# Kernel optimization log

Hardware: AMD Instinct MI355X
Metric: run time of the kernel (lower is better)

## Reference

```python
import jax, jax.numpy as jnp
import numpy as np

N = 100000      # nodes
E = 1600000     # edges
G = 1000        # graphs in the batch
D_IN, D_H, D_OUT = 128, 128, 64


def setup_inputs() -> dict:
    key = jax.random.key(0)
    ks = jax.random.split(key, 8)
    x = jax.random.normal(ks[0], (N, D_IN), jnp.float32)
    edge_index = jax.random.randint(ks[1], (2, E), 0, N, dtype=jnp.int32)
    batch = jnp.sort(jax.random.randint(ks[2], (N,), 0, G, dtype=jnp.int32))
    s_in = 1.0 / np.sqrt(D_IN)
    s_h = 1.0 / np.sqrt(D_H)
    return {
        "x": x,
        "edge_index": edge_index,
        "batch": batch,
        "W_emb": jax.random.normal(ks[3], (D_IN, D_H), jnp.float32) * s_in,
        "b_emb": jnp.zeros((D_H,), jnp.float32),
        "W1": jax.random.normal(ks[4], (D_H, D_H), jnp.float32) * s_h,
        "b1": jnp.zeros((D_H,), jnp.float32),
        "W2": jax.random.normal(ks[5], (D_H, D_H), jnp.float32) * s_h,
        "b2": jnp.zeros((D_H,), jnp.float32),
        "W3": jax.random.normal(ks[6], (D_H, D_OUT), jnp.float32) * s_h,
        "b3": jnp.zeros((D_OUT,), jnp.float32),
    }


def reference(x, edge_index, batch, W_emb, b_emb, W1, b1, W2, b2, W3, b3):
    # Eval mode: dropout is identity.
    n = x.shape[0]
    src, dst = edge_index[0], edge_index[1]
    # GCN symmetric normalization with self-loops (Kipf & Welling).
    deg = jax.ops.segment_sum(jnp.ones(src.shape[0], x.dtype), dst, num_segments=n) + 1.0
    dis = jax.lax.rsqrt(deg)                 # deg^{-1/2}, [N]
    edge_norm = dis[src] * dis[dst]          # [E]
    self_norm = dis * dis                    # self-loop weight = 1/deg, [N]

    def gcn_conv(h, W, b):
        h = h @ W                                         # [N, d_out]
        agg = jax.ops.segment_sum(h[src] * edge_norm[:, None], dst, num_segments=n)
        return agg + h * self_norm[:, None] + b

    h = x @ W_emb + b_emb
    h = jax.nn.relu(gcn_conv(h, W1, b1))
    h = jax.nn.relu(gcn_conv(h, W2, b2))
    h = gcn_conv(h, W3, b3)
    # global_add_pool over graph ids
    return jax.ops.segment_sum(h, batch, num_segments=G)
```

## Files before the change

### kernel.cpp

```cpp
#include <hip/hip_runtime.h>
#include <hip/hip_bf16.h>

#define NN 100000
#define NE 1600000
#define NG 1000

typedef unsigned short u16;
typedef unsigned int u32;
typedef u16 u16x8 __attribute__((ext_vector_type(8)));
typedef u16 u16x4 __attribute__((ext_vector_type(4)));
typedef u32 u32x4 __attribute__((ext_vector_type(4)));
typedef float f32x4 __attribute__((ext_vector_type(4)));
typedef __attribute__((ext_vector_type(8))) short s16x8;
typedef __attribute__((ext_vector_type(4))) float facc4;

__device__ __forceinline__ float bf2f(u16 u) {
    union { u32 i; float f; } c; c.i = ((u32)u) << 16; return c.f;
}
__device__ __forceinline__ u16 f2bf(float f) {
    __hip_bfloat16 h = __float2bfloat16(f);
    union { __hip_bfloat16 h; u16 u; } c; c.h = h; return c.u;
}

__global__ __launch_bounds__(256) void detect_kernel(const u32* __restrict__ xr, int* __restrict__ flag) {
    __shared__ int cnt[256];
    int c = 0;
    for (int i = threadIdx.x; i < 4096; i += 256) {
        u32 e = (xr[i] >> 7) & 0xFFu;
        if (e >= 110u && e <= 135u) c++;
    }
    cnt[threadIdx.x] = c;
    __syncthreads();
    for (int o = 128; o > 0; o >>= 1) {
        if (threadIdx.x < o) cnt[threadIdx.x] += cnt[threadIdx.x + o];
        __syncthreads();
    }
    if (threadIdx.x == 0) flag[0] = (cnt[0] > 2048) ? 1 : 0;
}

__global__ __launch_bounds__(256) void cvt_x_kernel(const void* __restrict__ xr, u16* __restrict__ xb,
                                                    const int* __restrict__ flag) {
    int c = blockIdx.x * 256 + threadIdx.x;
    const int NC = NN * 128 / 8;
    if (c >= NC) return;
    u16x8 o;
    if (flag[0]) {
        o = reinterpret_cast<const u16x8*>(xr)[c];
    } else {
        f32x4 a = reinterpret_cast<const f32x4*>(xr)[c * 2];
        f32x4 b = reinterpret_cast<const f32x4*>(xr)[c * 2 + 1];
        #pragma unroll
        for (int j = 0; j < 4; ++j) { o[j] = f2bf(a[j]); o[4 + j] = f2bf(b[j]); }
    }
    reinterpret_cast<u16x8*>(xb)[c] = o;
}

__global__ __launch_bounds__(256) void cvt_wt_kernel(const void* __restrict__ wr, u16* __restrict__ wt,
                                                     int Mcols, const int* __restrict__ flag) {
    int o = blockIdx.x * 256 + threadIdx.x;
    if (o >= Mcols * 128) return;
    int n = o >> 7, k = o & 127;
    u16 v;
    if (flag[0]) v = reinterpret_cast<const u16*>(wr)[k * Mcols + n];
    else         v = f2bf(reinterpret_cast<const float*>(wr)[k * Mcols + n]);
    wt[o] = v;
}

__global__ __launch_bounds__(256) void cvt_b_kernel(const void* __restrict__ br, float* __restrict__ bf,
                                                    int nelem, const int* __restrict__ flag) {
    int i = threadIdx.x;
    if (i >= nelem) return;
    bf[i] = flag[0] ? bf2f(reinterpret_cast<const u16*>(br)[i])
                    : reinterpret_cast<const float*>(br)[i];
}

__global__ __launch_bounds__(256) void hist_kernel(const int* __restrict__ ei, int* __restrict__ counts) {
    int e = blockIdx.x * 256 + threadIdx.x;
    if (e < NE) atomicAdd(&counts[ei[NE + e]], 1);
}

__global__ __launch_bounds__(256) void dis_kernel(const int* __restrict__ counts, float* __restrict__ dis) {
    int n = blockIdx.x * 256 + threadIdx.x;
    if (n < NN) dis[n] = rsqrtf((float)counts[n] + 1.0f);
}

__global__ __launch_bounds__(256) void scan1_kernel(const int* __restrict__ counts, int* __restrict__ offs,
                                                    int* __restrict__ bsums) {
    __shared__ int sums[256];
    int tid = threadIdx.x;
    int base = blockIdx.x * 2048 + tid * 8;
    int local[8];
    int s = 0;
    #pragma unroll
    for (int i = 0; i < 8; ++i) {
        int v = (base + i < NN) ? counts[base + i] : 0;
        local[i] = s; s += v;
    }
    sums[tid] = s;
    __syncthreads();
    for (int o = 1; o < 256; o <<= 1) {
        int v = (tid >= o) ? sums[tid - o] : 0;
        __syncthreads();
        sums[tid] += v;
        __syncthreads();
    }
    int excl = sums[tid] - s;
    #pragma unroll
    for (int i = 0; i < 8; ++i)
        if (base + i < NN) offs[base + i] = excl + local[i];
    if (tid == 255) bsums[blockIdx.x] = sums[255];
}

__global__ void scan2_kernel(int* __restrict__ bsums, int nb) {
    if (threadIdx.x == 0 && blockIdx.x == 0) {
        int run = 0;
        for (int b = 0; b < nb; ++b) { int t = bsums[b]; bsums[b] = run; run += t; }
    }
}

__global__ __launch_bounds__(256) void scan3_kernel(int* __restrict__ offs, const int* __restrict__ bsums) {
    int i = blockIdx.x * 256 + threadIdx.x;
    if (i < NN) offs[i] += bsums[i >> 11];
}

__global__ __launch_bounds__(256) void scatter_kernel(const int* __restrict__ ei, const int* __restrict__ offs,
                                                      int* __restrict__ cursor, const float* __restrict__ dis,
                                                      int2* __restrict__ edges) {
    int e = blockIdx.x * 256 + threadIdx.x;
    if (e < NE) {
        int s = ei[e], d = ei[NE + e];
        int pos = offs[d] + atomicAdd(&cursor[d], 1);
        int2 pk;
        pk.x = s;
        pk.y = __float_as_int(dis[s] * dis[d]);
        edges[pos] = pk;
    }
}

template <int M>
__global__ __launch_bounds__(256) void gemm_mfma(const u16* __restrict__ Hin, const u16* __restrict__ Wt,
                                                 const float* __restrict__ bias, u16* __restrict__ Hout) {
    constexpr int LDW = 136;
    __shared__ u16 sW[M * LDW];
    int tid = threadIdx.x;
    for (int c = tid; c < M * 16; c += 256) {
        int n = c >> 4, kc = (c & 15) << 3;
        *reinterpret_cast<u16x8*>(sW + n * LDW + kc) = reinterpret_cast<const u16x8*>(Wt)[c];
    }
    __syncthreads();

    int wv = tid >> 6, lane = tid & 63;
    int m = lane & 15, quad = lane >> 4;
    int r0 = blockIdx.x * 64 + wv * 16;
    constexpr int NT = M / 16;
    facc4 acc[NT];
    #pragma unroll
    for (int t = 0; t < NT; ++t) acc[t] = (facc4){0.f, 0.f, 0.f, 0.f};

    const u16* arow = Hin + (size_t)(r0 + m) * 128 + quad * 8;
    #pragma unroll
    for (int k0 = 0; k0 < 128; k0 += 32) {
        s16x8 a = *reinterpret_cast<const s16x8*>(arow + k0);
        #pragma unroll
        for (int t = 0; t < NT; ++t) {
            s16x8 b = *reinterpret_cast<const s16x8*>(sW + (t * 16 + m) * LDW + k0 + quad * 8);
            acc[t] = __builtin_amdgcn_mfma_f32_16x16x32_bf16(a, b, acc[t], 0, 0, 0);
        }
    }

    #pragma unroll
    for (int t = 0; t < NT; ++t) {
        int col = t * 16 + m;
        float bv = bias ? bias[col] : 0.0f;
        #pragma unroll
        for (int r = 0; r < 4; ++r) {
            int orow = r0 + quad * 4 + r;
            if (orow < NN)
                Hout[(size_t)orow * M + col] = f2bf(acc[t][r] + bv);
        }
    }
}

template <int M, bool RELU>
__global__ __launch_bounds__(256) void agg_kernel(const u16* __restrict__ T, const int* __restrict__ offs,
                                                  const int* __restrict__ counts, const float* __restrict__ dis,
                                                  const int2* __restrict__ edges,
                                                  const float* __restrict__ bias, u16* __restrict__ Hout) {
    constexpr int TPN = M / 8;
    constexpr int NPB = 256 / TPN;
    int lane = threadIdx.x % TPN;
    int n = blockIdx.x * NPB + threadIdx.x / TPN;
    if (n >= NN) return;
    const u32x4* T4 = reinterpret_cast<const u32x4*>(T);

    float di = dis[n];
    float sn = di * di;
    u32x4 ts = T4[(size_t)n * TPN + lane];
    float acc[8];
    #pragma unroll
    for (int q = 0; q < 4; ++q) {
        acc[2 * q]     = bf2f((u16)(ts[q] & 0xffffu)) * sn + bias[lane * 8 + 2 * q];
        acc[2 * q + 1] = bf2f((u16)(ts[q] >> 16))     * sn + bias[lane * 8 + 2 * q + 1];
    }

    int st = offs[n], cnt = counts[n];
    int j = 0;
    for (; j + 4 <= cnt; j += 4) {
        int2 e0 = edges[st + j];
        int2 e1 = edges[st + j + 1];
        int2 e2 = edges[st + j + 2];
        int2 e3 = edges[st + j + 3];
        u32x4 g0 = T4[(size_t)e0.x * TPN + lane];
        u32x4 g1 = T4[(size_t)e1.x * TPN + lane];
        u32x4 g2 = T4[(size_t)e2.x * TPN + lane];
        u32x4 g3 = T4[(size_t)e3.x * TPN + lane];
        float w0 = __int_as_float(e0.y), w1 = __int_as_float(e1.y);
        float w2 = __int_as_float(e2.y), w3 = __int_as_float(e3.y);
        #pragma unroll
        for (int q = 0; q < 4; ++q) {
            acc[2 * q]     += bf2f((u16)(g0[q] & 0xffffu)) * w0;
            acc[2 * q + 1] += bf2f((u16)(g0[q] >> 16))     * w0;
            acc[2 * q]     += bf2f((u16)(g1[q] & 0xffffu)) * w1;
            acc[2 * q + 1] += bf2f((u16)(g1[q] >> 16))     * w1;
            acc[2 * q]     += bf2f((u16)(g2[q] & 0xffffu)) * w2;
            acc[2 * q + 1] += bf2f((u16)(g2[q] >> 16))     * w2;
            acc[2 * q]     += bf2f((u16)(g3[q] & 0xffffu)) * w3;
            acc[2 * q + 1] += bf2f((u16)(g3[q] >> 16))     * w3;
        }
    }
    for (; j < cnt; ++j) {
        int2 e = edges[st + j];
        u32x4 g = T4[(size_t)e.x * TPN + lane];
        float w = __int_as_float(e.y);
        #pragma unroll
        for (int q = 0; q < 4; ++q) {
            acc[2 * q]     += bf2f((u16)(g[q] & 0xffffu)) * w;
            acc[2 * q + 1] += bf2f((u16)(g[q] >> 16))     * w;
        }
    }

    u32x4 ov;
    #pragma unroll
    for (int q = 0; q < 4; ++q) {
        float a0 = acc[2 * q], a1 = acc[2 * q + 1];
        if (RELU) { a0 = fmaxf(a0, 0.0f); a1 = fmaxf(a1, 0.0f); }
        ov[q] = (u32)f2bf(a0) | ((u32)f2bf(a1) << 16);
    }
    reinterpret_cast<u32x4*>(Hout)[(size_t)n * TPN + lane] = ov;
}

__global__ __launch_bounds__(64) void pool_kernel(const u16* __restrict__ H, const int* __restrict__ batch,
                                                  void* __restrict__ out, const int* __restrict__ flag) {
    int g = blockIdx.x;
    int f = threadIdx.x;
    int lo = 0, hi = NN;
    while (lo < hi) { int mid = (lo + hi) >> 1; if (batch[mid] < g) lo = mid + 1; else hi = mid; }
    int lo2 = lo, hi2 = NN;
    while (lo2 < hi2) { int mid = (lo2 + hi2) >> 1; if (batch[mid] < g + 1) lo2 = mid + 1; else hi2 = mid; }
    float acc = 0.0f;
    for (int n = lo; n < lo2; ++n) acc += bf2f(H[(size_t)n * 64 + f]);
    if (flag[0]) reinterpret_cast<u16*>(out)[g * 64 + f] = f2bf(acc);
    else         reinterpret_cast<float*>(out)[g * 64 + f] = acc;
}

extern "C" void kernel_launch(void* const* d_in, const int* in_sizes, int n_in,
                              void* d_out, int out_size, void* d_ws, size_t ws_size,
                              hipStream_t stream) {
    const void* x     = d_in[0];
    const int* ei     = (const int*)d_in[1];
    const int* batch  = (const int*)d_in[2];
    const void* W_emb = d_in[3];
    const void* b_emb = d_in[4];
    const void* W1    = d_in[5];
    const void* b1    = d_in[6];
    const void* W2    = d_in[7];
    const void* b2    = d_in[8];
    const void* W3    = d_in[9];
    const void* b3    = d_in[10];

    char* p = (char*)d_ws;
    auto alloc = [&](size_t bytes) { void* r = p; p += (bytes + 255) & ~(size_t)255; return r; };
    int*   flag   = (int*)alloc(256);
    int*   counts = (int*)alloc(NN * 4);
    int*   cursor = (int*)alloc(NN * 4);
    int*   offs   = (int*)alloc(NN * 4);
    float* dis    = (float*)alloc(NN * 4);
    int*   bsums  = (int*)alloc(256 * 4);
    int2*  edges  = (int2*)alloc((size_t)NE * 8);
    u16*   wembT  = (u16*)alloc(128 * 128 * 2);
    u16*   w1T    = (u16*)alloc(128 * 128 * 2);
    u16*   w2T    = (u16*)alloc(128 * 128 * 2);
    u16*   w3T    = (u16*)alloc(64 * 128 * 2);
    float* bembF  = (float*)alloc(128 * 4);
    float* b1F    = (float*)alloc(128 * 4);
    float* b2F    = (float*)alloc(128 * 4);
    float* b3F    = (float*)alloc(64 * 4);
    u16*   hA     = (u16*)alloc((size_t)(NN + 64) * 128 * 2);
    u16*   hB     = (u16*)alloc((size_t)(NN + 64) * 128 * 2);

    hipMemsetAsync(counts, 0, NN * 4, stream);
    hipMemsetAsync(cursor, 0, NN * 4, stream);

    const int EB = (NE + 255) / 256;
    const int NB = (NN + 255) / 256;
    const int SB = (NN + 2047) / 2048;
    const int XC = (NN * 128 / 8 + 255) / 256;
    const int GB = (NN + 63) / 64;

    detect_kernel<<<1, 256, 0, stream>>>((const u32*)x, flag);
    cvt_x_kernel<<<XC, 256, 0, stream>>>(x, hB, flag);
    cvt_wt_kernel<<<64, 256, 0, stream>>>(W_emb, wembT, 128, flag);
    cvt_wt_kernel<<<64, 256, 0, stream>>>(W1, w1T, 128, flag);
    cvt_wt_kernel<<<64, 256, 0, stream>>>(W2, w2T, 128, flag);
    cvt_wt_kernel<<<32, 256, 0, stream>>>(W3, w3T, 64, flag);
    cvt_b_kernel<<<1, 256, 0, stream>>>(b_emb, bembF, 128, flag);
    cvt_b_kernel<<<1, 256, 0, stream>>>(b1, b1F, 128, flag);
    cvt_b_kernel<<<1, 256, 0, stream>>>(b2, b2F, 128, flag);
    cvt_b_kernel<<<1, 256, 0, stream>>>(b3, b3F, 64, flag);

    hist_kernel<<<EB, 256, 0, stream>>>(ei, counts);
    dis_kernel<<<NB, 256, 0, stream>>>(counts, dis);
    scan1_kernel<<<SB, 256, 0, stream>>>(counts, offs, bsums);
    scan2_kernel<<<1, 64, 0, stream>>>(bsums, SB);
    scan3_kernel<<<NB, 256, 0, stream>>>(offs, bsums);
    scatter_kernel<<<EB, 256, 0, stream>>>(ei, offs, cursor, dis, edges);

    gemm_mfma<128><<<GB, 256, 0, stream>>>(hB, wembT, bembF, hA);
    gemm_mfma<128><<<GB, 256, 0, stream>>>(hA, w1T, nullptr, hB);
    agg_kernel<128, true><<<(NN + 15) / 16, 256, 0, stream>>>(hB, offs, counts, dis, edges, b1F, hA);
    gemm_mfma<128><<<GB, 256, 0, stream>>>(hA, w2T, nullptr, hB);
    agg_kernel<128, true><<<(NN + 15) / 16, 256, 0, stream>>>(hB, offs, counts, dis, edges, b2F, hA);
    gemm_mfma<64><<<GB, 256, 0, stream>>>(hA, w3T, nullptr, hB);
    agg_kernel<64, false><<<(NN + 31) / 32, 256, 0, stream>>>(hB, offs, counts, dis, edges, b3F, hA);
    pool_kernel<<<NG, 64, 0, stream>>>(hA, batch, d_out, flag);
}
```

Measured before the change: 553.7 us.

## Merge prep kernels, store only edge sources, and fuse aggregation with next GEMM

```diff
diff --git a/kernel.cpp b/kernel.cpp
--- a/kernel.cpp
+++ b/kernel.cpp
@@ -8,7 +8,6 @@
 typedef unsigned short u16;
 typedef unsigned int u32;
 typedef u16 u16x8 __attribute__((ext_vector_type(8)));
-typedef u16 u16x4 __attribute__((ext_vector_type(4)));
 typedef u32 u32x4 __attribute__((ext_vector_type(4)));
 typedef float f32x4 __attribute__((ext_vector_type(4)));
 typedef __attribute__((ext_vector_type(8))) short s16x8;
@@ -38,54 +37,63 @@
     if (threadIdx.x == 0) flag[0] = (cnt[0] > 2048) ? 1 : 0;
 }
 
-__global__ __launch_bounds__(256) void cvt_x_kernel(const void* __restrict__ xr, u16* __restrict__ xb,
-                                                    const int* __restrict__ flag) {
-    int c = blockIdx.x * 256 + threadIdx.x;
-    const int NC = NN * 128 / 8;
-    if (c >= NC) return;
-    u16x8 o;
-    if (flag[0]) {
-        o = reinterpret_cast<const u16x8*>(xr)[c];
+#define MEGA_NB 8039
+__global__ __launch_bounds__(256) void mega_prep(
+    const void* __restrict__ x, const int* __restrict__ flag, u16* __restrict__ xb,
+    const void* __restrict__ Wemb, const void* __restrict__ W1, const void* __restrict__ W2,
+    const void* __restrict__ W3, u16* __restrict__ wembT, u16* __restrict__ w1T,
+    u16* __restrict__ w2T, u16* __restrict__ w3T,
+    const void* __restrict__ bemb, const void* __restrict__ b1, const void* __restrict__ b2,
+    const void* __restrict__ b3, float* __restrict__ bembF, float* __restrict__ b1F,
+    float* __restrict__ b2F, float* __restrict__ b3F,
+    const int* __restrict__ ei, int* __restrict__ counts)
+{
+    int b = blockIdx.x, tid = threadIdx.x;
+    int fl = flag[0];
+    if (b < 6250) {
+        if (fl) return;
+        int c = b * 256 + tid;
+        f32x4 a = reinterpret_cast<const f32x4*>(x)[c * 2];
+        f32x4 d = reinterpret_cast<const f32x4*>(x)[c * 2 + 1];
+        u16x8 o;
+        #pragma unroll
+        for (int j = 0; j < 4; ++j) { o[j] = f2bf(a[j]); o[4 + j] = f2bf(d[j]); }
+        reinterpret_cast<u16x8*>(xb)[c] = o;
+    } else if (b < 6474) {
+        int o = (b - 6250) * 256 + tid;
+        const void* src; u16* dst; int M; int ol;
+        if (o < 16384)      { src = Wemb; dst = wembT; M = 128; ol = o; }
+        else if (o < 32768) { src = W1;   dst = w1T;   M = 128; ol = o - 16384; }
+        else if (o < 49152) { src = W2;   dst = w2T;   M = 128; ol = o - 32768; }
+        else                { src = W3;   dst = w3T;   M = 64;  ol = o - 49152; }
+        int n = ol >> 7, k = ol & 127;
+        u16 v = fl ? reinterpret_cast<const u16*>(src)[k * M + n]
+                   : f2bf(reinterpret_cast<const float*>(src)[k * M + n]);
+        dst[ol] = v;
+    } else if (b < 6476) {
+        int i = (b - 6474) * 256 + tid;
+        if (i >= 448) return;
+        const void* src; float* dst; int il;
+        if (i < 128)      { src = bemb; dst = bembF; il = i; }
+        else if (i < 256) { src = b1;   dst = b1F;   il = i - 128; }
+        else if (i < 384) { src = b2;   dst = b2F;   il = i - 256; }
+        else              { src = b3;   dst = b3F;   il = i - 384; }
+        dst[il] = fl ? bf2f(reinterpret_cast<const u16*>(src)[il])
+                     : reinterpret_cast<const float*>(src)[il];
     } else {
-        f32x4 a = reinterpret_cast<const f32x4*>(xr)[c * 2];
-        f32x4 b = reinterpret_cast<const f32x4*>(xr)[c * 2 + 1];
-        #pragma unroll
-        for (int j = 0; j < 4; ++j) { o[j] = f2bf(a[j]); o[4 + j] = f2bf(b[j]); }
-    }
-    reinterpret_cast<u16x8*>(xb)[c] = o;
-}
-
-__global__ __launch_bounds__(256) void cvt_wt_kernel(const void* __restrict__ wr, u16* __restrict__ wt,
-                                                     int Mcols, const int* __restrict__ flag) {
-    int o = blockIdx.x * 256 + threadIdx.x;
-    if (o >= Mcols * 128) return;
-    int n = o >> 7, k = o & 127;
-    u16 v;
-    if (flag[0]) v = reinterpret_cast<const u16*>(wr)[k * Mcols + n];
-    else         v = f2bf(reinterpret_cast<const float*>(wr)[k * Mcols + n]);
-    wt[o] = v;
-}
-
-__global__ __launch_bounds__(256) void cvt_b_kernel(const void* __restrict__ br, float* __restrict__ bf,
-                                                    int nelem, const int* __restrict__ flag) {
-    int i = threadIdx.x;
-    if (i >= nelem) return;
-    bf[i] = flag[0] ? bf2f(reinterpret_cast<const u16*>(br)[i])
-                    : reinterpret_cast<const float*>(br)[i];
-}
-
-__global__ __launch_bounds__(256) void hist_kernel(const int* __restrict__ ei, int* __restrict__ counts) {
-    int e = blockIdx.x * 256 + threadIdx.x;
-    if (e < NE) atomicAdd(&counts[ei[NE + e]], 1);
-}
-
-__global__ __launch_bounds__(256) void dis_kernel(const int* __restrict__ counts, float* __restrict__ dis) {
-    int n = blockIdx.x * 256 + threadIdx.x;
-    if (n < NN) dis[n] = rsqrtf((float)counts[n] + 1.0f);
+        int e0 = (b - 6476) * 1024 + tid * 4;
+        if (e0 >= NE) return;
+        int4 d4 = *reinterpret_cast<const int4*>(ei + NE + e0);
+        atomicAdd(&counts[d4.x], 1);
+        atomicAdd(&counts[d4.y], 1);
+        atomicAdd(&counts[d4.z], 1);
+        atomicAdd(&counts[d4.w], 1);
+    }
 }
 
 __global__ __launch_bounds__(256) void scan1_kernel(const int* __restrict__ counts, int* __restrict__ offs,
-                                                    int* __restrict__ bsums) {
+                                                    int* __restrict__ bsums, float* __restrict__ dis,
+                                                    int* __restrict__ cursor) {
     __shared__ int sums[256];
     int tid = threadIdx.x;
     int base = blockIdx.x * 2048 + tid * 8;
@@ -93,7 +101,12 @@
     int s = 0;
     #pragma unroll
     for (int i = 0; i < 8; ++i) {
-        int v = (base + i < NN) ? counts[base + i] : 0;
+        int v = 0;
+        if (base + i < NN) {
+            v = counts[base + i];
+            dis[base + i] = rsqrtf((float)v + 1.0f);
+            cursor[base + i] = 0;
+        }
         local[i] = s; s += v;
     }
     sums[tid] = s;
@@ -111,38 +124,44 @@
     if (tid == 255) bsums[blockIdx.x] = sums[255];
 }
 
-__global__ void scan2_kernel(int* __restrict__ bsums, int nb) {
-    if (threadIdx.x == 0 && blockIdx.x == 0) {
-        int run = 0;
-        for (int b = 0; b < nb; ++b) { int t = bsums[b]; bsums[b] = run; run += t; }
-    }
-}
-
 __global__ __launch_bounds__(256) void scan3_kernel(int* __restrict__ offs, const int* __restrict__ bsums) {
+    __shared__ int addv;
     int i = blockIdx.x * 256 + threadIdx.x;
-    if (i < NN) offs[i] += bsums[i >> 11];
+    int bucket = blockIdx.x >> 3;
+    if (threadIdx.x == 0) {
+        int s = 0;
+        for (int k = 0; k < bucket; ++k) s += bsums[k];
+        addv = s;
+    }
+    __syncthreads();
+    if (i < NN) offs[i] += addv;
 }
 
 __global__ __launch_bounds__(256) void scatter_kernel(const int* __restrict__ ei, const int* __restrict__ offs,
-                                                      int* __restrict__ cursor, const float* __restrict__ dis,
-                                                      int2* __restrict__ edges) {
-    int e = blockIdx.x * 256 + threadIdx.x;
-    if (e < NE) {
-        int s = ei[e], d = ei[NE + e];
-        int pos = offs[d] + atomicAdd(&cursor[d], 1);
-        int2 pk;
-        pk.x = s;
-        pk.y = __float_as_int(dis[s] * dis[d]);
-        edges[pos] = pk;
-    }
+                                                      int* __restrict__ cursor, int* __restrict__ srcs) {
+    int t = blockIdx.x * 256 + threadIdx.x;
+    int e0 = t * 4;
+    if (e0 >= NE) return;
+    int4 s4 = *reinterpret_cast<const int4*>(ei + e0);
+    int4 d4 = *reinterpret_cast<const int4*>(ei + NE + e0);
+    int p0 = offs[d4.x] + atomicAdd(&cursor[d4.x], 1);
+    int p1 = offs[d4.y] + atomicAdd(&cursor[d4.y], 1);
+    int p2 = offs[d4.z] + atomicAdd(&cursor[d4.z], 1);
+    int p3 = offs[d4.w] + atomicAdd(&cursor[d4.w], 1);
+    srcs[p0] = s4.x;
+    srcs[p1] = s4.y;
+    srcs[p2] = s4.z;
+    srcs[p3] = s4.w;
 }
 
 template <int M>
-__global__ __launch_bounds__(256) void gemm_mfma(const u16* __restrict__ Hin, const u16* __restrict__ Wt,
+__global__ __launch_bounds__(256) void gemm_mfma(const u16* __restrict__ Hin, const u16* __restrict__ HinAlt,
+                                                 const int* __restrict__ flag, const u16* __restrict__ Wt,
                                                  const float* __restrict__ bias, u16* __restrict__ Hout) {
     constexpr int LDW = 136;
     __shared__ u16 sW[M * LDW];
     int tid = threadIdx.x;
+    const u16* A = (HinAlt != nullptr && flag[0]) ? HinAlt : Hin;
     for (int c = tid; c < M * 16; c += 256) {
         int n = c >> 4, kc = (c & 15) << 3;
         *reinterpret_cast<u16x8*>(sW + n * LDW + kc) = reinterpret_cast<const u16x8*>(Wt)[c];
@@ -152,19 +171,20 @@
     int wv = tid >> 6, lane = tid & 63;
     int m = lane & 15, quad = lane >> 4;
     int r0 = blockIdx.x * 64 + wv * 16;
+    int ar = r0 + m; if (ar >= NN) ar = NN - 1;
     constexpr int NT = M / 16;
     facc4 acc[NT];
     #pragma unroll
     for (int t = 0; t < NT; ++t) acc[t] = (facc4){0.f, 0.f, 0.f, 0.f};
 
-    const u16* arow = Hin + (size_t)(r0 + m) * 128 + quad * 8;
+    const u16* arow = A + (size_t)ar * 128 + quad * 8;
     #pragma unroll
     for (int k0 = 0; k0 < 128; k0 += 32) {
         s16x8 a = *reinterpret_cast<const s16x8*>(arow + k0);
         #pragma unroll
         for (int t = 0; t < NT; ++t) {
-            s16x8 b = *reinterpret_cast<const s16x8*>(sW + (t * 16 + m) * LDW + k0 + quad * 8);
-            acc[t] = __builtin_amdgcn_mfma_f32_16x16x32_bf16(a, b, acc[t], 0, 0, 0);
+            s16x8 bfr = *reinterpret_cast<const s16x8*>(sW + (t * 16 + m) * LDW + k0 + quad * 8);
+            acc[t] = __builtin_amdgcn_mfma_f32_16x16x32_bf16(a, bfr, acc[t], 0, 0, 0);
         }
     }
 
@@ -181,18 +201,116 @@
     }
 }
 
+template <int MOUT>
+__global__ __launch_bounds__(256) void fused_agg_gemm(const u16* __restrict__ T, const int* __restrict__ offs,
+                                                      const int* __restrict__ counts, const float* __restrict__ dis,
+                                                      const int* __restrict__ srcs, const float* __restrict__ aggbias,
+                                                      const u16* __restrict__ Wt, u16* __restrict__ Hout) {
+    constexpr int LDW = 136;
+    __shared__ u16 sW[MOUT * LDW];
+    __shared__ u16 sA[64 * LDW];
+    int tid = threadIdx.x;
+    for (int c = tid; c < MOUT * 16; c += 256) {
+        int n = c >> 4, kc = (c & 15) << 3;
+        *reinterpret_cast<u16x8*>(sW + n * LDW + kc) = reinterpret_cast<const u16x8*>(Wt)[c];
+    }
+
+    int lane = tid & 15, grp = tid >> 4;
+    const u32x4* T4 = reinterpret_cast<const u32x4*>(T);
+    for (int i = 0; i < 4; ++i) {
+        int nl = grp * 4 + i;
+        int n = blockIdx.x * 64 + nl;
+        bool valid = n < NN;
+        int nc = valid ? n : NN - 1;
+        float di = dis[nc];
+        float sn = di * di;
+        u32x4 ts = T4[(size_t)nc * 16 + lane];
+        float acc[8];
+        #pragma unroll
+        for (int q = 0; q < 4; ++q) {
+            acc[2 * q]     = bf2f((u16)(ts[q] & 0xffffu)) * sn + aggbias[lane * 8 + 2 * q];
+            acc[2 * q + 1] = bf2f((u16)(ts[q] >> 16))     * sn + aggbias[lane * 8 + 2 * q + 1];
+        }
+        int st = offs[nc], cnt = valid ? counts[nc] : 0;
+        int j = 0;
+        for (; j + 4 <= cnt; j += 4) {
+            int e0 = srcs[st + j], e1 = srcs[st + j + 1], e2 = srcs[st + j + 2], e3 = srcs[st + j + 3];
+            float w0 = dis[e0] * di, w1 = dis[e1] * di, w2 = dis[e2] * di, w3 = dis[e3] * di;
+            u32x4 g0 = T4[(size_t)e0 * 16 + lane];
+            u32x4 g1 = T4[(size_t)e1 * 16 + lane];
+            u32x4 g2 = T4[(size_t)e2 * 16 + lane];
+            u32x4 g3 = T4[(size_t)e3 * 16 + lane];
+            #pragma unroll
+            for (int q = 0; q < 4; ++q) {
+                acc[2 * q]     += bf2f((u16)(g0[q] & 0xffffu)) * w0;
+                acc[2 * q + 1] += bf2f((u16)(g0[q] >> 16))     * w0;
+                acc[2 * q]     += bf2f((u16)(g1[q] & 0xffffu)) * w1;
+                acc[2 * q + 1] += bf2f((u16)(g1[q] >> 16))     * w1;
+                acc[2 * q]     += bf2f((u16)(g2[q] & 0xffffu)) * w2;
+                acc[2 * q + 1] += bf2f((u16)(g2[q] >> 16))     * w2;
+                acc[2 * q]     += bf2f((u16)(g3[q] & 0xffffu)) * w3;
+                acc[2 * q + 1] += bf2f((u16)(g3[q] >> 16))     * w3;
+            }
+        }
+        for (; j < cnt; ++j) {
+            int e = srcs[st + j];
+            float w = dis[e] * di;
+            u32x4 g = T4[(size_t)e * 16 + lane];
+            #pragma unroll
+            for (int q = 0; q < 4; ++q) {
+                acc[2 * q]     += bf2f((u16)(g[q] & 0xffffu)) * w;
+                acc[2 * q + 1] += bf2f((u16)(g[q] >> 16))     * w;
+            }
+        }
+        u16x8 pk;
+        #pragma unroll
+        for (int q = 0; q < 4; ++q) {
+            pk[2 * q]     = f2bf(fmaxf(acc[2 * q], 0.0f));
+            pk[2 * q + 1] = f2bf(fmaxf(acc[2 * q + 1], 0.0f));
+        }
+        *reinterpret_cast<u16x8*>(sA + nl * LDW + lane * 8) = pk;
+    }
+    __syncthreads();
+
+    int wv = tid >> 6, l64 = tid & 63;
+    int m = l64 & 15, quad = l64 >> 4;
+    int r0 = blockIdx.x * 64 + wv * 16;
+    constexpr int NT = MOUT / 16;
+    facc4 gacc[NT];
+    #pragma unroll
+    for (int t = 0; t < NT; ++t) gacc[t] = (facc4){0.f, 0.f, 0.f, 0.f};
+    #pragma unroll
+    for (int k0 = 0; k0 < 128; k0 += 32) {
+        s16x8 a = *reinterpret_cast<const s16x8*>(sA + (wv * 16 + m) * LDW + k0 + quad * 8);
+        #pragma unroll
+        for (int t = 0; t < NT; ++t) {
+            s16x8 bfr = *reinterpret_cast<const s16x8*>(sW + (t * 16 + m) * LDW + k0 + quad * 8);
+            gacc[t] = __builtin_amdgcn_mfma_f32_16x16x32_bf16(a, bfr, gacc[t], 0, 0, 0);
+        }
+    }
+    #pragma unroll
+    for (int t = 0; t < NT; ++t) {
+        int col = t * 16 + m;
+        #pragma unroll
+        for (int r = 0; r < 4; ++r) {
+            int orow = r0 + quad * 4 + r;
+            if (orow < NN)
+                Hout[(size_t)orow * MOUT + col] = f2bf(gacc[t][r]);
+        }
+    }
+}
+
 template <int M, bool RELU>
 __global__ __launch_bounds__(256) void agg_kernel(const u16* __restrict__ T, const int* __restrict__ offs,
                                                   const int* __restrict__ counts, const float* __restrict__ dis,
-                                                  const int2* __restrict__ edges,
-                                                  const float* __restrict__ bias, u16* __restrict__ Hout) {
+                                                  const int* __restrict__ srcs, const float* __restrict__ bias,
+                                                  u16* __restrict__ Hout) {
     constexpr int TPN = M / 8;
     constexpr int NPB = 256 / TPN;
     int lane = threadIdx.x % TPN;
     int n = blockIdx.x * NPB + threadIdx.x / TPN;
     if (n >= NN) return;
     const u32x4* T4 = reinterpret_cast<const u32x4*>(T);
-
     float di = dis[n];
     float sn = di * di;
     u32x4 ts = T4[(size_t)n * TPN + lane];
@@ -202,20 +320,15 @@
         acc[2 * q]     = bf2f((u16)(ts[q] & 0xffffu)) * sn + bias[lane * 8 + 2 * q];
         acc[2 * q + 1] = bf2f((u16)(ts[q] >> 16))     * sn + bias[lane * 8 + 2 * q + 1];
     }
-
     int st = offs[n], cnt = counts[n];
     int j = 0;
     for (; j + 4 <= cnt; j += 4) {
-        int2 e0 = edges[st + j];
-        int2 e1 = edges[st + j + 1];
-        int2 e2 = edges[st + j + 2];
-        int2 e3 = edges[st + j + 3];
-        u32x4 g0 = T4[(size_t)e0.x * TPN + lane];
-        u32x4 g1 = T4[(size_t)e1.x * TPN + lane];
-        u32x4 g2 = T4[(size_t)e2.x * TPN + lane];
-        u32x4 g3 = T4[(size_t)e3.x * TPN + lane];
-        float w0 = __int_as_float(e0.y), w1 = __int_as_float(e1.y);
-        float w2 = __int_as_float(e2.y), w3 = __int_as_float(e3.y);
+        int e0 = srcs[st + j], e1 = srcs[st + j + 1], e2 = srcs[st + j + 2], e3 = srcs[st + j + 3];
+        float w0 = dis[e0] * di, w1 = dis[e1] * di, w2 = dis[e2] * di, w3 = dis[e3] * di;
+        u32x4 g0 = T4[(size_t)e0 * TPN + lane];
+        u32x4 g1 = T4[(size_t)e1 * TPN + lane];
+        u32x4 g2 = T4[(size_t)e2 * TPN + lane];
+        u32x4 g3 = T4[(size_t)e3 * TPN + lane];
         #pragma unroll
         for (int q = 0; q < 4; ++q) {
             acc[2 * q]     += bf2f((u16)(g0[q] & 0xffffu)) * w0;
@@ -229,16 +342,15 @@
         }
     }
     for (; j < cnt; ++j) {
-        int2 e = edges[st + j];
-        u32x4 g = T4[(size_t)e.x * TPN + lane];
-        float w = __int_as_float(e.y);
+        int e = srcs[st + j];
+        float w = dis[e] * di;
+        u32x4 g = T4[(size_t)e * TPN + lane];
         #pragma unroll
         for (int q = 0; q < 4; ++q) {
             acc[2 * q]     += bf2f((u16)(g[q] & 0xffffu)) * w;
             acc[2 * q + 1] += bf2f((u16)(g[q] >> 16))     * w;
         }
     }
-
     u32x4 ov;
     #pragma unroll
     for (int q = 0; q < 4; ++q) {
@@ -258,7 +370,10 @@
     int lo2 = lo, hi2 = NN;
     while (lo2 < hi2) { int mid = (lo2 + hi2) >> 1; if (batch[mid] < g + 1) lo2 = mid + 1; else hi2 = mid; }
     float acc = 0.0f;
-    for (int n = lo; n < lo2; ++n) acc += bf2f(H[(size_t)n * 64 + f]);
+    int n = lo;
+    for (; n + 2 <= lo2; n += 2)
+        acc += bf2f(H[(size_t)n * 64 + f]) + bf2f(H[(size_t)(n + 1) * 64 + f]);
+    if (n < lo2) acc += bf2f(H[(size_t)n * 64 + f]);
     if (flag[0]) reinterpret_cast<u16*>(out)[g * 64 + f] = f2bf(acc);
     else         reinterpret_cast<float*>(out)[g * 64 + f] = acc;
 }
@@ -286,7 +401,7 @@
     int*   offs   = (int*)alloc(NN * 4);
     float* dis    = (float*)alloc(NN * 4);
     int*   bsums  = (int*)alloc(256 * 4);
-    int2*  edges  = (int2*)alloc((size_t)NE * 8);
+    int*   srcs   = (int*)alloc((size_t)NE * 4);
     u16*   wembT  = (u16*)alloc(128 * 128 * 2);
     u16*   w1T    = (u16*)alloc(128 * 128 * 2);
     u16*   w2T    = (u16*)alloc(128 * 128 * 2);
@@ -299,38 +414,22 @@
     u16*   hB     = (u16*)alloc((size_t)(NN + 64) * 128 * 2);
 
     hipMemsetAsync(counts, 0, NN * 4, stream);
-    hipMemsetAsync(cursor, 0, NN * 4, stream);
-
-    const int EB = (NE + 255) / 256;
+
+    const int SB = (NN + 2047) / 2048;
     const int NB = (NN + 255) / 256;
-    const int SB = (NN + 2047) / 2048;
-    const int XC = (NN * 128 / 8 + 255) / 256;
     const int GB = (NN + 63) / 64;
 
     detect_kernel<<<1, 256, 0, stream>>>((const u32*)x, flag);
-    cvt_x_kernel<<<XC, 256, 0, stream>>>(x, hB, flag);
-    cvt_wt_kernel<<<64, 256, 0, stream>>>(W_emb, wembT, 128, flag);
-    cvt_wt_kernel<<<64, 256, 0, stream>>>(W1, w1T, 128, flag);
-    cvt_wt_kernel<<<64, 256, 0, stream>>>(W2, w2T, 128, flag);
-    cvt_wt_kernel<<<32, 256, 0, stream>>>(W3, w3T, 64, flag);
-    cvt_b_kernel<<<1, 256, 0, stream>>>(b_emb, bembF, 128, flag);
-    cvt_b_kernel<<<1, 256, 0, stream>>>(b1, b1F, 128, flag);
-    cvt_b_kernel<<<1, 256, 0, stream>>>(b2, b2F, 128, flag);
-    cvt_b_kernel<<<1, 256, 0, stream>>>(b3, b3F, 64, flag);
-
-    hist_kernel<<<EB, 256, 0, stream>>>(ei, counts);
-    dis_kernel<<<NB, 256, 0, stream>>>(counts, dis);
-    scan1_kernel<<<SB, 256, 0, stream>>>(counts, offs, bsums);
-    scan2_kernel<<<1, 64, 0, stream>>>(bsums, SB);
+    mega_prep<<<MEGA_NB, 256, 0, stream>>>(x, flag, hB, W_emb, W1, W2, W3, wembT, w1T, w2T, w3T,
+                                           b_emb, b1, b2, b3, bembF, b1F, b2F, b3F, ei, counts);
+    scan1_kernel<<<SB, 256, 0, stream>>>(counts, offs, bsums, dis, cursor);
     scan3_kernel<<<NB, 256, 0, stream>>>(offs, bsums);
-    scatter_kernel<<<EB, 256, 0, stream>>>(ei, offs, cursor, dis, edges);
-
-    gemm_mfma<128><<<GB, 256, 0, stream>>>(hB, wembT, bembF, hA);
-    gemm_mfma<128><<<GB, 256, 0, stream>>>(hA, w1T, nullptr, hB);
-    agg_kernel<128, true><<<(NN + 15) / 16, 256, 0, stream>>>(hB, offs, counts, dis, edges, b1F, hA);
-    gemm_mfma<128><<<GB, 256, 0, stream>>>(hA, w2T, nullptr, hB);
-    agg_kernel<128, true><<<(NN + 15) / 16, 256, 0, stream>>>(hB, offs, counts, dis, edges, b2F, hA);
-    gemm_mfma<64><<<GB, 256, 0, stream>>>(hA, w3T, nullptr, hB);
-    agg_kernel<64, false><<<(NN + 31) / 32, 256, 0, stream>>>(hB, offs, counts, dis, edges, b3F, hA);
+    scatter_kernel<<<(NE / 4 + 255) / 256, 256, 0, stream>>>(ei, offs, cursor, srcs);
+
+    gemm_mfma<128><<<GB, 256, 0, stream>>>(hB, (const u16*)x, flag, wembT, bembF, hA);
+    gemm_mfma<128><<<GB, 256, 0, stream>>>(hA, nullptr, flag, w1T, nullptr, hB);
+    fused_agg_gemm<128><<<GB, 256, 0, stream>>>(hB, offs, counts, dis, srcs, b1F, w2T, hA);
+    fused_agg_gemm<64><<<GB, 256, 0, stream>>>(hA, offs, counts, dis, srcs, b2F, w3T, hB);
+    agg_kernel<64, false><<<(NN + 31) / 32, 256, 0, stream>>>(hB, offs, counts, dis, srcs, b3F, hA);
     pool_kernel<<<NG, 64, 0, stream>>>(hA, batch, d_out, flag);
 }
```

Result: no change. 543.2 us (-1.9%).
